# Optimization experiments

Hardware: AMD Instinct MI355X
Metric: run time of the kernel (lower is better)

Reference implementation:

```python
import jax, jax.numpy as jnp
import numpy as np

B, S, D, H = 4, 2048, 512, 8
DK = D // H
SCALE = 1.0 / np.sqrt(DK)


def setup_inputs() -> dict:
    key = jax.random.key(0)
    kx, kq, kk, kv = jax.random.split(key, 4)
    w_std = np.sqrt(2.0 / (D + D))  # xavier-ish scale
    return {
        "x": jax.random.normal(kx, (B, S, D), dtype=jnp.float32),
        "W_Q": jax.random.normal(kq, (D, D), dtype=jnp.float32) * w_std,
        "W_K": jax.random.normal(kk, (D, D), dtype=jnp.float32) * w_std,
        "W_V": jax.random.normal(kv, (D, D), dtype=jnp.float32) * w_std,
    }


def reference(x, W_Q, W_K, W_V):
    # torch Linear(bias=False): y = x @ W.T
    q = jnp.einsum('bsd,ed->bse', x, W_Q).reshape(B, S, H, DK).transpose(0, 2, 1, 3)
    k = jnp.einsum('bsd,ed->bse', x, W_K).reshape(B, S, H, DK).transpose(0, 2, 1, 3)
    v = jnp.einsum('bsd,ed->bse', x, W_V).reshape(B, S, H, DK).transpose(0, 2, 1, 3)
    scores = jnp.einsum('bhqd,bhkd->bhqk', q, k) * SCALE  # [B,H,S,S]
    scores_exp = jnp.exp(scores)  # faithful: no max-subtraction in original
    attn = scores_exp / (scores_exp.sum(axis=-1, keepdims=True) + 1e-8)
    context = jnp.einsum('bhqk,bhkd->bhqd', attn, v)
    return context.transpose(0, 2, 1, 3).reshape(B, S, D)
```

## Files before the change

kernel.cpp:

```cpp
#include <hip/hip_runtime.h>
#include <hip/hip_bf16.h>

#define Bsz 4
#define Ssz 2048
#define Dsz 512
#define Hsz 8
#define DKsz 64

typedef __bf16 bf16x8 __attribute__((ext_vector_type(8)));
typedef __bf16 bf16x4 __attribute__((ext_vector_type(4)));
typedef float f32x4 __attribute__((ext_vector_type(4)));

#define SWE(c, row) ((((c) ^ ((row) & 7)) * 8))

__global__ __launch_bounds__(256) void cvt_kernel(
    const float* __restrict__ x, const float* __restrict__ Wq,
    const float* __restrict__ Wk, const float* __restrict__ Wv,
    __bf16* __restrict__ xb, __bf16* __restrict__ Wb)
{
    const int i = blockIdx.x * 256 + threadIdx.x;
    const int XN4 = (Bsz * Ssz * Dsz) / 4;
    const float* src;
    __bf16* dst;
    int off;
    if (i < XN4) {
        src = x; dst = xb; off = i;
    } else {
        int j = i - XN4;
        int w = j >> 16;
        off = j & 65535;
        src = (w == 0) ? Wq : (w == 1) ? Wk : Wv;
        dst = Wb + (size_t)w * (Dsz * Dsz);
    }
    float4 v = ((const float4*)src)[off];
    __bf16 o[4] = {(__bf16)v.x, (__bf16)v.y, (__bf16)v.z, (__bf16)v.w};
    *(uint2*)(dst + (size_t)off * 4) = *(uint2*)o;
}

__global__ __launch_bounds__(256, 3) void qkv_kernel(
    const __bf16* __restrict__ xb, const __bf16* __restrict__ Wb,
    __bf16* __restrict__ Qo, __bf16* __restrict__ Ko, __bf16* __restrict__ Vo)
{
    __shared__ __bf16 xs[128][64];
    __shared__ __bf16 wsh[128][64];

    const int tid  = threadIdx.x;
    const int lane = tid & 63;
    const int wave = tid >> 6;
    const int quad = lane >> 4;
    const int l16  = lane & 15;
    const int wm   = (wave & 1) * 64;
    const int wn   = (wave >> 1) * 64;

    const int lin = blockIdx.x;
    const int xcd = lin & 7;
    const int idx = lin >> 3;
    const int tnw = idx % 12;
    const int tmh = idx / 12;
    const int tm  = (tmh * 8 + xcd) * 128;
    const int tn  = (tnw & 3) * 128;
    const int which = tnw >> 2;
    const bool VM = (which == 2);
    const __bf16* W = Wb + (size_t)which * (Dsz * Dsz);

    const int srow = tid >> 3;
    const int sc   = tid & 7;
    const int swz  = SWE(sc, srow);

    const __bf16* xg = xb + (size_t)(tm + srow) * Dsz + sc * 8;
    const __bf16* wg = W  + (size_t)(tn + srow) * Dsz + sc * 8;

    bf16x8 px[4], pw[4];
    #pragma unroll
    for (int i = 0; i < 4; ++i) {
        px[i] = *(const bf16x8*)(xg + (size_t)(32 * i) * Dsz);
        pw[i] = *(const bf16x8*)(wg + (size_t)(32 * i) * Dsz);
    }

    f32x4 acc[4][4];
    #pragma unroll
    for (int i = 0; i < 4; ++i)
        #pragma unroll
        for (int j = 0; j < 4; ++j) acc[i][j] = (f32x4){0.f, 0.f, 0.f, 0.f};

    const __bf16 (*Ash)[64] = VM ? xs : wsh;
    const __bf16 (*Bsh)[64] = VM ? wsh : xs;

    for (int k0 = 0; k0 < Dsz; k0 += 64) {
        __syncthreads();
        #pragma unroll
        for (int i = 0; i < 4; ++i) {
            *(bf16x8*)&xs[srow + 32 * i][swz]  = px[i];
            *(bf16x8*)&wsh[srow + 32 * i][swz] = pw[i];
        }
        __syncthreads();
        if (k0 + 64 < Dsz) {
            #pragma unroll
            for (int i = 0; i < 4; ++i) {
                px[i] = *(const bf16x8*)(xg + (size_t)(32 * i) * Dsz + k0 + 64);
                pw[i] = *(const bf16x8*)(wg + (size_t)(32 * i) * Dsz + k0 + 64);
            }
        }

        #pragma unroll
        for (int kk = 0; kk < 2; ++kk) {
            bf16x8 fa[4], fb[4];
            #pragma unroll
            for (int mi = 0; mi < 4; ++mi) {
                const int row = wm + mi * 16 + l16;
                fa[mi] = *(const bf16x8*)&Ash[row][SWE(kk * 4 + quad, row)];
            }
            #pragma unroll
            for (int ni = 0; ni < 4; ++ni) {
                const int row = wn + ni * 16 + l16;
                fb[ni] = *(const bf16x8*)&Bsh[row][SWE(kk * 4 + quad, row)];
            }
            #pragma unroll
            for (int mi = 0; mi < 4; ++mi)
                #pragma unroll
                for (int ni = 0; ni < 4; ++ni)
                    acc[mi][ni] = __builtin_amdgcn_mfma_f32_16x16x32_bf16(
                        fa[mi], fb[ni], acc[mi][ni], 0, 0, 0);
        }
    }

    if (!VM) {
        const float scale = (which == 0) ? 0.125f * 1.44269504088896340736f : 1.0f;
        __bf16* dst = (which == 0) ? Qo : Ko;
        #pragma unroll
        for (int mi = 0; mi < 4; ++mi) {
            const int e0 = tn + wm + mi * 16 + quad * 4;
            const int h = e0 >> 6, d0 = e0 & 63;
            #pragma unroll
            for (int ni = 0; ni < 4; ++ni) {
                const int sf = tm + wn + ni * 16 + l16;
                const int b = sf >> 11, s = sf & (Ssz - 1);
                bf16x4 p;
                #pragma unroll
                for (int r = 0; r < 4; ++r) p[r] = (__bf16)(acc[mi][ni][r] * scale);
                *(bf16x4*)&dst[((((size_t)(b * Hsz + h) * Ssz + s)) << 6) + d0] = p;
            }
        }
    } else {
        #pragma unroll
        for (int mi = 0; mi < 4; ++mi) {
            const int sf0 = tm + wm + mi * 16 + quad * 4;
            const int b = sf0 >> 11, s0 = sf0 & (Ssz - 1);
            #pragma unroll
            for (int ni = 0; ni < 4; ++ni) {
                const int e = tn + wn + ni * 16 + l16;
                const int h = e >> 6, d = e & 63;
                bf16x4 p;
                #pragma unroll
                for (int r = 0; r < 4; ++r) p[r] = (__bf16)acc[mi][ni][r];
                *(bf16x4*)&Vo[(((size_t)(b * Hsz + h) * DKsz + d) << 11) + s0] = p;
            }
        }
    }
}

__global__ __launch_bounds__(256, 2) void attn_kernel(
    const __bf16* __restrict__ Q, const __bf16* __restrict__ K,
    const __bf16* __restrict__ VT, float* __restrict__ out)
{
    __shared__ __bf16 ks[64][64];
    __shared__ __bf16 vs[64][64];
    __shared__ __bf16 ps[4][16][64];

    const int tid  = threadIdx.x;
    const int lane = tid & 63;
    const int wave = tid >> 6;
    const int quad = lane >> 4;
    const int l16  = lane & 15;

    const int bh = blockIdx.x;
    const int qt = blockIdx.y;
    const int b  = bh >> 3;
    const int h  = bh & 7;

    const __bf16* Qb = Q  + (size_t)bh * Ssz * DKsz;
    const __bf16* Kb = K  + (size_t)bh * Ssz * DKsz;
    const __bf16* Vb = VT + (size_t)bh * DKsz * Ssz;

    bf16x8 qf[2][2];
    #pragma unroll
    for (int qs = 0; qs < 2; ++qs) {
        const __bf16* qrow = Qb + (size_t)(qt * 128 + wave * 32 + qs * 16 + l16) * DKsz;
        qf[qs][0] = *(const bf16x8*)(qrow + quad * 8);
        qf[qs][1] = *(const bf16x8*)(qrow + 32 + quad * 8);
    }

    bf16x8 ones;
    #pragma unroll
    for (int i = 0; i < 8; ++i) ones[i] = (__bf16)1.0f;

    f32x4 oacc[2][4];
    #pragma unroll
    for (int qs = 0; qs < 2; ++qs)
        #pragma unroll
        for (int i = 0; i < 4; ++i) oacc[qs][i] = (f32x4){0.f, 0.f, 0.f, 0.f};
    f32x4 lacc[2] = {(f32x4){0.f, 0.f, 0.f, 0.f}, (f32x4){0.f, 0.f, 0.f, 0.f}};

    const int srow = tid >> 3;
    const int sc   = tid & 7;
    const int swz  = SWE(sc, srow);

    const __bf16* kg = Kb + (size_t)srow * DKsz + sc * 8;
    const __bf16* vg = Vb + (size_t)srow * Ssz + sc * 8;

    bf16x8 pk0 = *(const bf16x8*)(kg);
    bf16x8 pk1 = *(const bf16x8*)(kg + (size_t)32 * DKsz);
    bf16x8 pv0 = *(const bf16x8*)(vg);
    bf16x8 pv1 = *(const bf16x8*)(vg + (size_t)32 * Ssz);

    for (int kb = 0; kb < Ssz; kb += 64) {
        __syncthreads();
        *(bf16x8*)&ks[srow][swz]      = pk0;
        *(bf16x8*)&ks[srow + 32][swz] = pk1;
        *(bf16x8*)&vs[srow][swz]      = pv0;
        *(bf16x8*)&vs[srow + 32][swz] = pv1;
        __syncthreads();

        if (kb + 64 < Ssz) {
            pk0 = *(const bf16x8*)(kg + (size_t)(kb + 64) * DKsz);
            pk1 = *(const bf16x8*)(kg + (size_t)(kb + 96) * DKsz);
            pv0 = *(const bf16x8*)(vg + kb + 64);
            pv1 = *(const bf16x8*)(vg + (size_t)32 * Ssz + kb + 64);
        }

        bf16x8 kf[2][4], vf[2][4];
        #pragma unroll
        for (int kk = 0; kk < 2; ++kk)
            #pragma unroll
            for (int ns = 0; ns < 4; ++ns) {
                const int row = ns * 16 + l16;
                kf[kk][ns] = *(const bf16x8*)&ks[row][SWE(kk * 4 + quad, row)];
                vf[kk][ns] = *(const bf16x8*)&vs[row][SWE(kk * 4 + quad, row)];
            }

        #pragma unroll
        for (int qs = 0; qs < 2; ++qs) {
            #pragma unroll
            for (int ns = 0; ns < 4; ++ns) {
                f32x4 st = (f32x4){0.f, 0.f, 0.f, 0.f};
                st = __builtin_amdgcn_mfma_f32_16x16x32_bf16(kf[0][ns], qf[qs][0], st, 0, 0, 0);
                st = __builtin_amdgcn_mfma_f32_16x16x32_bf16(kf[1][ns], qf[qs][1], st, 0, 0, 0);
                bf16x4 pp;
                #pragma unroll
                for (int r = 0; r < 4; ++r)
                    pp[r] = (__bf16)__builtin_amdgcn_exp2f(st[r]);
                const int c = ns * 2 + (quad >> 1);
                *(bf16x4*)&ps[wave][l16][((c ^ (l16 & 7)) << 3) + ((quad & 1) << 2)] = pp;
            }
            bf16x8 af0 = *(const bf16x8*)&ps[wave][l16][SWE(quad, l16)];
            bf16x8 af1 = *(const bf16x8*)&ps[wave][l16][SWE(4 + quad, l16)];
            #pragma unroll
            for (int ns = 0; ns < 4; ++ns) {
                oacc[qs][ns] = __builtin_amdgcn_mfma_f32_16x16x32_bf16(vf[0][ns], af0, oacc[qs][ns], 0, 0, 0);
                oacc[qs][ns] = __builtin_amdgcn_mfma_f32_16x16x32_bf16(vf[1][ns], af1, oacc[qs][ns], 0, 0, 0);
            }
            lacc[qs] = __builtin_amdgcn_mfma_f32_16x16x32_bf16(ones, af0, lacc[qs], 0, 0, 0);
            lacc[qs] = __builtin_amdgcn_mfma_f32_16x16x32_bf16(ones, af1, lacc[qs], 0, 0, 0);
        }
    }

    #pragma unroll
    for (int qs = 0; qs < 2; ++qs) {
        const float linv = 1.f / (lacc[qs][0] + 1e-8f);
        const int q = qt * 128 + wave * 32 + qs * 16 + l16;
        float* obase = out + ((size_t)b * Ssz + q) * Dsz + h * DKsz;
        #pragma unroll
        for (int ns = 0; ns < 4; ++ns) {
            f32x4 o = oacc[qs][ns] * linv;
            *(f32x4*)(obase + ns * 16 + quad * 4) = o;
        }
    }
}

extern "C" void kernel_launch(void* const* d_in, const int* in_sizes, int n_in,
                              void* d_out, int out_size, void* d_ws, size_t ws_size,
                              hipStream_t stream) {
    const float* x  = (const float*)d_in[0];
    const float* Wq = (const float*)d_in[1];
    const float* Wk = (const float*)d_in[2];
    const float* Wv = (const float*)d_in[3];
    float* out = (float*)d_out;

    const size_t per = (size_t)Bsz * Hsz * Ssz * DKsz;
    __bf16* Qw  = (__bf16*)d_ws;
    __bf16* Kw  = Qw + per;
    __bf16* VTw = Kw + per;
    __bf16* xb  = VTw + per;
    __bf16* Wb  = xb + per;

    cvt_kernel<<<4864, 256, 0, stream>>>(x, Wq, Wk, Wv, xb, Wb);
    qkv_kernel<<<768, 256, 0, stream>>>(xb, Wb, Qw, Kw, VTw);
    attn_kernel<<<dim3(Bsz * Hsz, Ssz / 128), 256, 0, stream>>>(Qw, Kw, VTw, out);
}
```

Baseline: 137.2 us.

## Use two waves per attention block with 64 query rows each

Shrinks the attention block from four waves to two, and each wave now handles 64 query rows (four 16-row sub-tiles) instead of 32. K/V tile staging is redistributed so each thread loads four rows instead of two. This reuses the K/V fragments read from shared memory across more queries, cutting LDS traffic per MFMA. The cost is more registers per thread for accumulators and fewer waves per block to hide latency.

```diff
diff --git a/kernel.cpp b/kernel.cpp
--- a/kernel.cpp
+++ b/kernel.cpp
@@ -159,13 +159,13 @@
     }
 }
 
-__global__ __launch_bounds__(256, 2) void attn_kernel(
+__global__ __launch_bounds__(128, 2) void attn_kernel(
     const __bf16* __restrict__ Q, const __bf16* __restrict__ K,
     const __bf16* __restrict__ VT, float* __restrict__ out)
 {
     __shared__ __bf16 ks[64][64];
     __shared__ __bf16 vs[64][64];
-    __shared__ __bf16 ps[4][16][64];
+    __shared__ __bf16 ps[2][16][64];
 
     const int tid  = threadIdx.x;
     const int lane = tid & 63;
@@ -182,10 +182,10 @@
     const __bf16* Kb = K  + (size_t)bh * Ssz * DKsz;
     const __bf16* Vb = VT + (size_t)bh * DKsz * Ssz;
 
-    bf16x8 qf[2][2];
-    #pragma unroll
-    for (int qs = 0; qs < 2; ++qs) {
-        const __bf16* qrow = Qb + (size_t)(qt * 128 + wave * 32 + qs * 16 + l16) * DKsz;
+    bf16x8 qf[4][2];
+    #pragma unroll
+    for (int qs = 0; qs < 4; ++qs) {
+        const __bf16* qrow = Qb + (size_t)(qt * 128 + wave * 64 + qs * 16 + l16) * DKsz;
         qf[qs][0] = *(const bf16x8*)(qrow + quad * 8);
         qf[qs][1] = *(const bf16x8*)(qrow + 32 + quad * 8);
     }
@@ -194,12 +194,14 @@
     #pragma unroll
     for (int i = 0; i < 8; ++i) ones[i] = (__bf16)1.0f;
 
-    f32x4 oacc[2][4];
-    #pragma unroll
-    for (int qs = 0; qs < 2; ++qs)
+    f32x4 oacc[4][4];
+    #pragma unroll
+    for (int qs = 0; qs < 4; ++qs)
         #pragma unroll
         for (int i = 0; i < 4; ++i) oacc[qs][i] = (f32x4){0.f, 0.f, 0.f, 0.f};
-    f32x4 lacc[2] = {(f32x4){0.f, 0.f, 0.f, 0.f}, (f32x4){0.f, 0.f, 0.f, 0.f}};
+    f32x4 lacc[4];
+    #pragma unroll
+    for (int qs = 0; qs < 4; ++qs) lacc[qs] = (f32x4){0.f, 0.f, 0.f, 0.f};
 
     const int srow = tid >> 3;
     const int sc   = tid & 7;
@@ -208,24 +210,28 @@
     const __bf16* kg = Kb + (size_t)srow * DKsz + sc * 8;
     const __bf16* vg = Vb + (size_t)srow * Ssz + sc * 8;
 
-    bf16x8 pk0 = *(const bf16x8*)(kg);
-    bf16x8 pk1 = *(const bf16x8*)(kg + (size_t)32 * DKsz);
-    bf16x8 pv0 = *(const bf16x8*)(vg);
-    bf16x8 pv1 = *(const bf16x8*)(vg + (size_t)32 * Ssz);
+    bf16x8 pk[4], pv[4];
+    #pragma unroll
+    for (int i = 0; i < 4; ++i) {
+        pk[i] = *(const bf16x8*)(kg + (size_t)(16 * i) * DKsz);
+        pv[i] = *(const bf16x8*)(vg + (size_t)(16 * i) * Ssz);
+    }
 
     for (int kb = 0; kb < Ssz; kb += 64) {
         __syncthreads();
-        *(bf16x8*)&ks[srow][swz]      = pk0;
-        *(bf16x8*)&ks[srow + 32][swz] = pk1;
-        *(bf16x8*)&vs[srow][swz]      = pv0;
-        *(bf16x8*)&vs[srow + 32][swz] = pv1;
+        #pragma unroll
+        for (int i = 0; i < 4; ++i) {
+            *(bf16x8*)&ks[srow + 16 * i][swz] = pk[i];
+            *(bf16x8*)&vs[srow + 16 * i][swz] = pv[i];
+        }
         __syncthreads();
 
         if (kb + 64 < Ssz) {
-            pk0 = *(const bf16x8*)(kg + (size_t)(kb + 64) * DKsz);
-            pk1 = *(const bf16x8*)(kg + (size_t)(kb + 96) * DKsz);
-            pv0 = *(const bf16x8*)(vg + kb + 64);
-            pv1 = *(const bf16x8*)(vg + (size_t)32 * Ssz + kb + 64);
+            #pragma unroll
+            for (int i = 0; i < 4; ++i) {
+                pk[i] = *(const bf16x8*)(kg + (size_t)(kb + 64 + 16 * i) * DKsz);
+                pv[i] = *(const bf16x8*)(vg + (size_t)(16 * i) * Ssz + kb + 64);
+            }
         }
 
         bf16x8 kf[2][4], vf[2][4];
@@ -239,7 +245,7 @@
             }
 
         #pragma unroll
-        for (int qs = 0; qs < 2; ++qs) {
+        for (int qs = 0; qs < 4; ++qs) {
             #pragma unroll
             for (int ns = 0; ns < 4; ++ns) {
                 f32x4 st = (f32x4){0.f, 0.f, 0.f, 0.f};
@@ -265,9 +271,9 @@
     }
 
     #pragma unroll
-    for (int qs = 0; qs < 2; ++qs) {
+    for (int qs = 0; qs < 4; ++qs) {
         const float linv = 1.f / (lacc[qs][0] + 1e-8f);
-        const int q = qt * 128 + wave * 32 + qs * 16 + l16;
+        const int q = qt * 128 + wave * 64 + qs * 16 + l16;
         float* obase = out + ((size_t)b * Ssz + q) * Dsz + h * DKsz;
         #pragma unroll
         for (int ns = 0; ns < 4; ++ns) {
@@ -295,5 +301,5 @@
 
     cvt_kernel<<<4864, 256, 0, stream>>>(x, Wq, Wk, Wv, xb, Wb);
     qkv_kernel<<<768, 256, 0, stream>>>(xb, Wb, Qw, Kw, VTw);
-    attn_kernel<<<dim3(Bsz * Hsz, Ssz / 128), 256, 0, stream>>>(Qw, Kw, VTw, out);
+    attn_kernel<<<dim3(Bsz * Hsz, Ssz / 128), 128, 0, stream>>>(Qw, Kw, VTw, out);
 }
```

Result: slower. 156.6 us (+14.1%).
